# Kernel tuning notes

Measured on AMD Instinct MI355X. Metric: run time of the kernel, lower is better.

Reference implementation:

```python
import jax, jax.numpy as jnp
import numpy as np
from jax import lax

INPUT_SIZE = 16384
NUM_CONV = 128
KMAX = 11  # max kernel size from {7, 9, 11}
BATCH = 256


def setup_inputs() -> dict:
    # Mirror FeatureExtractor._generate_random_params / _generate_random_convolutions
    rng = np.random.RandomState(0)
    kernel_sizes = rng.choice([7, 9, 11], NUM_CONV)
    dilations, paddings = [], []
    W = np.zeros((NUM_CONV, KMAX), np.float32)  # zero-padded kernel bank
    b = np.zeros((NUM_CONV,), np.float32)
    for i, k in enumerate(kernel_sizes):
        d_f = 2.0 ** rng.uniform(0.0, np.log2((INPUT_SIZE - 1) / (k - 1)))
        p = (k - 1) * d_f // 2 if rng.randint(2) else 0
        dilations.append(int(d_f))
        paddings.append(int(p))
        w = rng.normal(0.0, 1.0, k)
        w = w - w.mean()  # centered kernel ('normal' sampling type)
        W[i, :k] = w.astype(np.float32)
        b[i] = rng.uniform(-1.0, 1.0)
    key = jax.random.key(0)
    x = jax.random.normal(key, (BATCH, 1, INPUT_SIZE), dtype=jnp.float32)
    return {
        "x": x,
        "weights": jnp.asarray(W),
        "biases": jnp.asarray(b),
        "kernel_sizes": np.asarray(kernel_sizes, np.int64),
        "dilations": np.asarray(dilations, np.int64),
        "paddings": np.asarray(paddings, np.int64),
    }


def reference(x, weights, biases, kernel_sizes, dilations, paddings):
    # x: [B, 1, L]. Each conv has its own (k, dilation, padding) -> distinct
    # output lengths, so a Python loop over the fixed NUM_CONV structurally
    # distinct convs is required (matches the original module).
    feats = []
    n = weights.shape[0]
    for i in range(n):
        k = int(kernel_sizes[i])
        d = int(dilations[i])
        p = int(paddings[i])
        w = weights[i, :k].reshape(1, 1, k)  # OIW
        # torch Conv1d = cross-correlation with rhs (kernel) dilation
        y = lax.conv_general_dilated(
            x, w, window_strides=(1,), padding=[(p, p)], rhs_dilation=(d,)
        ) + biases[i]
        fm = y[:, 0, :]                      # [B, L_out]
        mx = fm.max(axis=-1)                 # global max pool
        ppv = (fm >= 0).sum(axis=-1) / fm.shape[-1]  # proportion of positives
        feats.append(jnp.stack([mx, ppv.astype(x.dtype)], axis=-1))  # [B, 2]
    out = jnp.concatenate(feats, axis=-1)    # [B, 2*num_conv], interleaved (max, ppv)
    return out.reshape(out.shape[0], 1, out.shape[1])  # [B, 1, 2*num_conv]
```

## Files before the change

kernel.cpp:

```cpp
#include <hip/hip_runtime.h>
#include <math.h>

#define S_LEN   16384
#define NCONV   128
#define NBATCH  256
#define TPB     1024
#define NGRP    8
#define DSTRIDE 24
#define BIGQ    (1 << 28)
#define CLMP    65552u

typedef float __attribute__((address_space(1))) as1_float;
typedef float __attribute__((address_space(3))) as3_float;
typedef __attribute__((ext_vector_type(2))) float f2;
typedef unsigned long long u64;

__global__ void setup_desc(const int* __restrict__ ks, const int* __restrict__ dil,
                           const int* __restrict__ pad, const float* __restrict__ W,
                           const float* __restrict__ bias, int* __restrict__ ws)
{
  __shared__ int cost_s[NCONV];
  __shared__ int grp_s[NCONV];
  const int ci = threadIdx.x;
  const int is64 = (ks[1] == 0);
  const int k = is64 ? ks[2 * ci]  : ks[ci];
  const int d = is64 ? dil[2 * ci] : dil[ci];
  const int p = is64 ? pad[2 * ci] : pad[ci];
  const int L = S_LEN + 2 * p - d * (k - 1);
  const int A = L / d, B = L - A * d;
  int cost = L * (k + 5) + ((d >= 128) ? (d >> 1) : 64) * (k - 1) * 2;
  if (d == 1) cost = L * (k + 5) * 2;
  cost_s[ci] = cost;
  __syncthreads();
  int rank = 0;
  for (int j = 0; j < NCONV; ++j) {
    const int cj = cost_s[j];
    rank += (cj > cost) || (cj == cost && j < ci);
  }
  int gg = rank & 7;
  if ((rank >> 3) & 1) gg = 7 - gg;
  grp_s[ci] = gg;
  __syncthreads();
  int rho = 0;
  for (int j = 0; j < NCONV; ++j) {
    if (grp_s[j] != gg) continue;
    const int cj = cost_s[j];
    rho += (cj > cost) || (cj == cost && j < ci);
  }
#pragma unroll
  for (int h = 0; h < 2; ++h) {
    const int j2 = 2 * rho + h;
    const int wv = (j2 < 16) ? j2 : 31 - j2;
    const int sq = (j2 < 16) ? 0 : 1;
    int* dsc = ws + (gg * 32 + wv * 2 + sq) * DSTRIDE;
    dsc[0] = d; dsc[1] = p; dsc[2] = A; dsc[3] = B;
    dsc[4] = ci; dsc[5] = rho; dsc[6] = h; dsc[7] = k;
    ((float*)dsc)[8] = 1.0f / (float)L;
    ((float*)dsc)[9] = bias[ci];
#pragma unroll
    for (int t = 0; t < 11; ++t) ((float*)dsc)[10 + t] = W[ci * 11 + t];
  }
}

__device__ __forceinline__ float sgpr_f(float v) {
  return __int_as_float(__builtin_amdgcn_readfirstlane(__float_as_int(v)));
}
__device__ __forceinline__ int sgpr_i(int v) {
  return __builtin_amdgcn_readfirstlane(v);
}
__device__ __forceinline__ float rcpf(float x) { return __builtin_amdgcn_rcpf(x); }

__device__ __forceinline__ int divq(int num, float rd, int d) {
  int q = (int)((float)num * rd);
  q -= (q * d > num);
  q += ((q + 1) * d <= num);
  return q;
}

__device__ __forceinline__ f2 rd2b(const float* sh, int ib) {
  unsigned u = (unsigned)ib;
  u = u > CLMP ? CLMP : u;
  const float* p = (const float*)((const char*)sh + u);
  f2 v; v.x = p[0]; v.y = p[1];
  return v;
}
__device__ __forceinline__ float ld1b(const float* sh, int ib) {
  unsigned u = (unsigned)ib;
  u = u > CLMP ? CLMP : u;
  return *(const float*)((const char*)sh + u);
}

__device__ __forceinline__ f2 pfma(f2 a, f2 b, f2 c) {
#if __has_builtin(__builtin_elementwise_fma)
  return __builtin_elementwise_fma(a, b, c);
#else
  f2 r; r.x = fmaf(a.x, b.x, c.x); r.y = fmaf(a.y, b.y, c.y); return r;
#endif
}
__device__ __forceinline__ f2 pmax(f2 a, f2 b) {
#if __has_builtin(__builtin_elementwise_max)
  return __builtin_elementwise_max(a, b);
#else
  f2 r; r.x = fmaxf(a.x, b.x); r.y = fmaxf(a.y, b.y); return r;
#endif
}
__device__ __forceinline__ int wcount(bool pred) {
  return (int)__popcll(__ballot(pred));
}

template <int K>
__device__ __forceinline__ void pwalk(
    const float* sh, const u64* wu, const f2 bbv,
    int d, int sb4, int q0, int q1, f2& mxv, int& cw)
{
  const int n = q1 - q0;
  if (n <= 0) return;
  f2 win[K];
  int bb = (sb4 + q0 * d) * 4;
#pragma unroll
  for (int t = 0; t < K - 1; ++t)
    win[t] = rd2b(sh, bb + t * (d * 4));
  bb += (K - 1) * (d * 4);
  int i = 0;
  for (; i + K <= n; i += K) {
#pragma unroll
    for (int s = 0; s < K; ++s) {
      const f2 cur = rd2b(sh, bb + s * (d * 4));
      f2 a = pfma(__builtin_bit_cast(f2, wu[0]), win[s % K], bbv);
#pragma unroll
      for (int t = 1; t < K; ++t)
        a = pfma(__builtin_bit_cast(f2, wu[t]),
                 (t == K - 1) ? cur : win[(s + t) % K], a);
      win[(s + K - 1) % K] = cur;
      mxv = pmax(mxv, a);
      cw += wcount(a.x >= 0.f);
      cw += wcount(a.y >= 0.f);
    }
    bb += K * (d * 4);
  }
  const int rem = n - i;
  if (rem > 0) {
#pragma unroll
    for (int s = 0; s < K - 1; ++s) {
      const f2 cur = rd2b(sh, bb + s * (d * 4));
      f2 a = pfma(__builtin_bit_cast(f2, wu[0]), win[s % K], bbv);
#pragma unroll
      for (int t = 1; t < K; ++t)
        a = pfma(__builtin_bit_cast(f2, wu[t]),
                 (t == K - 1) ? cur : win[(s + t) % K], a);
      win[(s + K - 1) % K] = cur;
      const bool ok = (s < rem);
      if (ok) mxv = pmax(mxv, a);
      cw += wcount(ok && (a.x >= 0.f));
      cw += wcount(ok && (a.y >= 0.f));
    }
  }
}

template <int K>
__device__ __forceinline__ void swalk(
    const float* sh, const float* w, float bval,
    int d, int sb4, int q0, int q1, float& mx, int& cw)
{
  const int n = q1 - q0;
  if (n <= 0) return;
  float win[K];
  int bb = (sb4 + q0 * d) * 4;
#pragma unroll
  for (int t = 0; t < K - 1; ++t)
    win[t] = ld1b(sh, bb + t * (d * 4));
  bb += (K - 1) * (d * 4);
  int i = 0;
  for (; i + K <= n; i += K) {
#pragma unroll
    for (int s = 0; s < K; ++s) {
      const float cur = ld1b(sh, bb + s * (d * 4));
      float a = fmaf(w[0], win[s % K], bval);
#pragma unroll
      for (int t = 1; t < K; ++t)
        a = fmaf(w[t], (t == K - 1) ? cur : win[(s + t) % K], a);
      win[(s + K - 1) % K] = cur;
      mx = fmaxf(mx, a);
      cw += wcount(a >= 0.f);
    }
    bb += K * (d * 4);
  }
  const int rem = n - i;
  if (rem > 0) {
#pragma unroll
    for (int s = 0; s < K - 1; ++s) {
      const float cur = ld1b(sh, bb + s * (d * 4));
      float a = fmaf(w[0], win[s % K], bval);
#pragma unroll
      for (int t = 1; t < K; ++t)
        a = fmaf(w[t], (t == K - 1) ? cur : win[(s + t) % K], a);
      win[(s + K - 1) % K] = cur;
      const bool ok = (s < rem);
      if (ok) mx = fmaxf(mx, a);
      cw += wcount(ok && (a >= 0.f));
    }
  }
}

template <int K>
__device__ __forceinline__ void scalar_split(
    const float* sh, const float* w, float bval,
    int d, int p, int r, int c0, int c1, int lane, float& mx, int& cw)
{
  const int n = c1 - c0;
  if (n <= 0) return;
  const int v  = lane;
  const int mm = n >> 6;
  const int sA = (mm >= 32) ? (v & 31) : (((v & 31) * mm) >> 5);
  const int vB = v + 1;
  const int sB = (mm >= 32) ? (vB & 31) : (((vB & 31) * mm) >> 5);
  const int q0 = c0 + (int)(((long long)n * v) >> 6) + sA;
  const int q1 = (v == 63) ? c1 : c0 + (int)(((long long)n * vB) >> 6) + sB;
  swalk<K>(sh, w, bval, d, r - p + 4, q0, q1, mx, cw);
}

template <int K>
__device__ __forceinline__ void one_out(
    const float* sh, const float* w, float bval,
    int d, int p, int j, float& mx, int& cw)
{
  float a = bval;
  int bb = (j - p + 4) * 4;
#pragma unroll
  for (int t = 0; t < K; ++t) { a = fmaf(w[t], ld1b(sh, bb), a); bb += d * 4; }
  mx = fmaxf(mx, a);
  cw += wcount(a >= 0.f);
}

template <int K>
__device__ __forceinline__ void conv_chunk(
    const float* sh, const u64* wu, const float* w, float bval, const f2 bbv,
    int d, int p, int A, int B, int h, int lane,
    f2& mxv, float& mxs, int& cw)
{
  if (d == 1) {
    const int H = (A + 1) >> 1;
    scalar_split<K>(sh, w, bval, 1, p, 0, h ? H : 0, h ? A : H, lane, mxs, cw);
    return;
  }
  const int npair = d >> 1;
  if (npair >= 128) {
    const int half = npair >> 1;
    const int g0 = h ? half : 0;
    const int g1 = h ? npair : half;
    for (int c = g0 + lane; c < g1; c += 64) {
      const int r0 = 2 * c;
      const int Qm = A + (r0 + 1 < B);
      pwalk<K>(sh, wu, bbv, d, r0 - p + 4, 0, Qm, mxv, cw);
      if (B == r0 + 1) one_out<K>(sh, w, bval, d, p, r0 + A * d, mxs, cw);
    }
  } else if (npair >= 64) {
    const int H = (A + 1) >> 1;
    const int c0 = h ? H : 0;
    const int c1 = h ? BIGQ : H;
    for (int c = lane; c < npair; c += 64) {
      const int r0 = 2 * c;
      const int Qm = A + (r0 + 1 < B);
      pwalk<K>(sh, wu, bbv, d, r0 - p + 4, c0, min(c1, Qm), mxv, cw);
      if (B == r0 + 1 && A >= c0 && A < c1)
        one_out<K>(sh, w, bval, d, p, r0 + A * d, mxs, cw);
    }
  } else {
    const int H = (A + 1) >> 1;
    const int c0 = h ? H : 0;
    const int c1h = h ? BIGQ : H;
    const float rdp = rcpf((float)npair);
    int v  = (int)((float)lane * rdp);
    int g2 = lane - v * npair;
    if (g2 < 0)           { --v; g2 += npair; }
    else if (g2 >= npair) { ++v; g2 -= npair; }
    const int nv = divq(63 - g2, rdp, npair) + 1;
    const int r0 = 2 * g2;
    const int Qm = A + (r0 + 1 < B);
    const int cc1 = min(c1h, Qm);
    const int n = cc1 - c0;
    if (n > 0) {
      const float rn = rcpf((float)nv);
      const int mm = (int)((float)n * rn);
      const int sA = (mm >= 32) ? (v & 31) : (((v & 31) * mm) >> 5);
      const int vB = v + 1;
      const int sB = (mm >= 32) ? (vB & 31) : (((vB & 31) * mm) >> 5);
      const int q0 = c0 + (int)((float)(n * v) * rn) + sA;
      const int q1 = (v == nv - 1) ? cc1
                   : c0 + (int)((float)(n * vB) * rn) + sB;
      pwalk<K>(sh, wu, bbv, d, r0 - p + 4, q0, q1, mxv, cw);
    }
    if (v == nv - 1 && B == r0 + 1 && A >= c0 && A < c1h)
      one_out<K>(sh, w, bval, d, p, r0 + A * d, mxs, cw);
  }
  if ((d & 1) && d > 1) {
    const int H2 = (A + 1) >> 1;
    const int r = d - 1;
    const int Qr = A + (r < B);
    const int c0 = h ? H2 : 0;
    const int c1 = h ? Qr : min(H2, Qr);
    scalar_split<K>(sh, w, bval, d, p, r, c0, c1, lane, mxs, cw);
  }
}

__global__ __launch_bounds__(TPB, 8) void rocket_feats(
    const float* __restrict__ x, const int* __restrict__ ws,
    float* __restrict__ out)
{
  __shared__ float sh[S_LEN + 8];
  __shared__ float smx[2][16];
  __shared__ int   scn[2][16];
  __shared__ int   sci[16];
  __shared__ float sin_[16];

  const int tid  = threadIdx.x;
  const int blk  = blockIdx.x;
  const int g    = blk & 7;
  const int b    = blk >> 3;
  const int lane = tid & 63, wid = tid >> 6;

  const float* xrow = x + (size_t)b * S_LEN;
  {
    const float* gb = xrow + lane * 4;
#pragma unroll
    for (int c = 0; c < 4; ++c) {
      const int off = (wid * 4 + c) * 256;
      __builtin_amdgcn_global_load_lds((const as1_float*)(gb + off),
                                       (as3_float*)(sh + 4 + off), 16, 0, 0);
    }
  }
  if (tid < 4) sh[tid] = 0.f;
  if (tid >= 4 && tid < 8) sh[S_LEN + tid] = 0.f;
  __syncthreads();

  for (int sq = 0; sq < 2; ++sq) {
    const int* dsc = ws + (g * 32 + wid * 2 + sq) * DSTRIDE;
    const int d  = sgpr_i(dsc[0]);
    const int p  = sgpr_i(dsc[1]);
    const int A  = sgpr_i(dsc[2]);
    const int B  = sgpr_i(dsc[3]);
    const int ci = sgpr_i(dsc[4]);
    const int t_ = sgpr_i(dsc[5]);
    const int h  = sgpr_i(dsc[6]);
    const int k  = sgpr_i(dsc[7]);
    const float invL = sgpr_f(((const float*)dsc)[8]);
    const float bval = sgpr_f(((const float*)dsc)[9]);
    float wf[11]; u64 wu[11];
#pragma unroll
    for (int t = 0; t < 11; ++t) {
      wf[t] = sgpr_f(((const float*)dsc)[10 + t]);
      const unsigned wb = (unsigned)__float_as_int(wf[t]);
      wu[t] = ((u64)wb << 32) | (u64)wb;
    }
    f2 bbv; bbv.x = bval; bbv.y = bval;

    f2 mxv; mxv.x = -INFINITY; mxv.y = -INFINITY;
    float mxs = -INFINITY;
    int cw = 0;

    if (k == 7)
      conv_chunk<7 >(sh, wu, wf, bval, bbv, d, p, A, B, h, lane, mxv, mxs, cw);
    else if (k == 9)
      conv_chunk<9 >(sh, wu, wf, bval, bbv, d, p, A, B, h, lane, mxv, mxs, cw);
    else
      conv_chunk<11>(sh, wu, wf, bval, bbv, d, p, A, B, h, lane, mxv, mxs, cw);

    float mx = fmaxf(fmaxf(mxv.x, mxv.y), mxs);
#pragma unroll
    for (int off = 32; off > 0; off >>= 1)
      mx = fmaxf(mx, __shfl_down(mx, off, 64));
    if (lane == 0) {
      smx[h][t_] = mx; scn[h][t_] = cw;
      sci[t_] = ci; sin_[t_] = invL;
    }
  }

  __syncthreads();
  if (tid < 16) {
    const float m = fmaxf(smx[0][tid], smx[1][tid]);
    const int   c = scn[0][tid] + scn[1][tid];
    out[(size_t)b * (2 * NCONV) + 2 * sci[tid]]     = m;
    out[(size_t)b * (2 * NCONV) + 2 * sci[tid] + 1] = (float)c * sin_[tid];
  }
}

extern "C" void kernel_launch(void* const* d_in, const int* in_sizes, int n_in,
                              void* d_out, int out_size, void* d_ws, size_t ws_size,
                              hipStream_t stream) {
  const float* x    = (const float*)d_in[0];
  const float* W    = (const float*)d_in[1];
  const float* bias = (const float*)d_in[2];
  const int*   ks   = (const int*)d_in[3];
  const int*   dil  = (const int*)d_in[4];
  const int*   pad  = (const int*)d_in[5];
  float* out = (float*)d_out;
  int*   ws  = (int*)d_ws;

  hipLaunchKernelGGL(setup_desc, dim3(1), dim3(NCONV), 0, stream,
                     ks, dil, pad, W, bias, ws);
  hipLaunchKernelGGL(rocket_feats, dim3(NBATCH * NGRP), dim3(TPB), 0, stream,
                     x, ws, out);
}
```

Baseline: 272.6 us.

## Process four dilated residue streams per lane with quad walk

Replaces the pair-of-residues walk for dilated convolutions with a quad walk that computes four adjacent residue streams per lane using two packed-FMA accumulators. It adds a pair/scalar split for the leftover residues and for dilations 2 and 3, and updates the cost model used for load balancing. The aim is to amortize LDS address computation and loop overhead over more outputs and to raise ILP. In exchange it doubles register pressure for the sliding windows, which could hurt occupancy, and it changes how work is divided across lanes for mid-range dilations.

New measurement: 316.1 us. 15.9% more time.

```diff
diff --git a/kernel.cpp b/kernel.cpp
--- a/kernel.cpp
+++ b/kernel.cpp
@@ -28,8 +28,8 @@
   const int p = is64 ? pad[2 * ci] : pad[ci];
   const int L = S_LEN + 2 * p - d * (k - 1);
   const int A = L / d, B = L - A * d;
-  int cost = L * (k + 5) + ((d >= 128) ? (d >> 1) : 64) * (k - 1) * 2;
-  if (d == 1) cost = L * (k + 5) * 2;
+  int cost = L * (k + 5) + ((d >= 512) ? (d >> 2) : 64) * (k - 1) * 4;
+  if (d < 4) cost = L * (k + 5) * 2;
   cost_s[ci] = cost;
   __syncthreads();
   int rank = 0;
@@ -158,8 +158,76 @@
 }
 
 template <int K>
+__device__ __forceinline__ void qwalk(
+    const float* sh, const u64* wu, const f2 bbv,
+    int d, int sb4, int q0, int q1, f2& mxv, int& cw)
+{
+  const int n = q1 - q0;
+  if (n <= 0) return;
+  f2 wlo[K], whi[K];
+  int bb = (sb4 + q0 * d) * 4;
+#pragma unroll
+  for (int t = 0; t < K - 1; ++t) {
+    wlo[t] = rd2b(sh, bb + t * (d * 4));
+    whi[t] = rd2b(sh, bb + t * (d * 4) + 8);
+  }
+  bb += (K - 1) * (d * 4);
+  int i = 0;
+  for (; i + K <= n; i += K) {
+#pragma unroll
+    for (int s = 0; s < K; ++s) {
+      const f2 clo = rd2b(sh, bb + s * (d * 4));
+      const f2 chi = rd2b(sh, bb + s * (d * 4) + 8);
+      f2 alo = pfma(__builtin_bit_cast(f2, wu[0]), wlo[s % K], bbv);
+      f2 ahi = pfma(__builtin_bit_cast(f2, wu[0]), whi[s % K], bbv);
+#pragma unroll
+      for (int t = 1; t < K; ++t) {
+        alo = pfma(__builtin_bit_cast(f2, wu[t]),
+                   (t == K - 1) ? clo : wlo[(s + t) % K], alo);
+        ahi = pfma(__builtin_bit_cast(f2, wu[t]),
+                   (t == K - 1) ? chi : whi[(s + t) % K], ahi);
+      }
+      wlo[(s + K - 1) % K] = clo;
+      whi[(s + K - 1) % K] = chi;
+      mxv = pmax(mxv, alo);
+      mxv = pmax(mxv, ahi);
+      cw += wcount(alo.x >= 0.f);
+      cw += wcount(alo.y >= 0.f);
+      cw += wcount(ahi.x >= 0.f);
+      cw += wcount(ahi.y >= 0.f);
+    }
+    bb += K * (d * 4);
+  }
+  const int rem = n - i;
+  if (rem > 0) {
+#pragma unroll
+    for (int s = 0; s < K - 1; ++s) {
+      const f2 clo = rd2b(sh, bb + s * (d * 4));
+      const f2 chi = rd2b(sh, bb + s * (d * 4) + 8);
+      f2 alo = pfma(__builtin_bit_cast(f2, wu[0]), wlo[s % K], bbv);
+      f2 ahi = pfma(__builtin_bit_cast(f2, wu[0]), whi[s % K], bbv);
+#pragma unroll
+      for (int t = 1; t < K; ++t) {
+        alo = pfma(__builtin_bit_cast(f2, wu[t]),
+                   (t == K - 1) ? clo : wlo[(s + t) % K], alo);
+        ahi = pfma(__builtin_bit_cast(f2, wu[t]),
+                   (t == K - 1) ? chi : whi[(s + t) % K], ahi);
+      }
+      wlo[(s + K - 1) % K] = clo;
+      whi[(s + K - 1) % K] = chi;
+      const bool ok = (s < rem);
+      if (ok) { mxv = pmax(mxv, alo); mxv = pmax(mxv, ahi); }
+      cw += wcount(ok && (alo.x >= 0.f));
+      cw += wcount(ok && (alo.y >= 0.f));
+      cw += wcount(ok && (ahi.x >= 0.f));
+      cw += wcount(ok && (ahi.y >= 0.f));
+    }
+  }
+}
+
+template <int K>
 __device__ __forceinline__ void swalk(
-    const float* sh, const float* w, float bval,
+    const float* sh, const float* wf, float bval,
     int d, int sb4, int q0, int q1, float& mx, int& cw)
 {
   const int n = q1 - q0;
@@ -175,10 +243,10 @@
 #pragma unroll
     for (int s = 0; s < K; ++s) {
       const float cur = ld1b(sh, bb + s * (d * 4));
-      float a = fmaf(w[0], win[s % K], bval);
+      float a = fmaf(wf[0], win[s % K], bval);
 #pragma unroll
       for (int t = 1; t < K; ++t)
-        a = fmaf(w[t], (t == K - 1) ? cur : win[(s + t) % K], a);
+        a = fmaf(wf[t], (t == K - 1) ? cur : win[(s + t) % K], a);
       win[(s + K - 1) % K] = cur;
       mx = fmaxf(mx, a);
       cw += wcount(a >= 0.f);
@@ -190,10 +258,10 @@
 #pragma unroll
     for (int s = 0; s < K - 1; ++s) {
       const float cur = ld1b(sh, bb + s * (d * 4));
-      float a = fmaf(w[0], win[s % K], bval);
+      float a = fmaf(wf[0], win[s % K], bval);
 #pragma unroll
       for (int t = 1; t < K; ++t)
-        a = fmaf(w[t], (t == K - 1) ? cur : win[(s + t) % K], a);
+        a = fmaf(wf[t], (t == K - 1) ? cur : win[(s + t) % K], a);
       win[(s + K - 1) % K] = cur;
       const bool ok = (s < rem);
       if (ok) mx = fmaxf(mx, a);
@@ -204,7 +272,7 @@
 
 template <int K>
 __device__ __forceinline__ void scalar_split(
-    const float* sh, const float* w, float bval,
+    const float* sh, const float* wf, float bval,
     int d, int p, int r, int c0, int c1, int lane, float& mx, int& cw)
 {
   const int n = c1 - c0;
@@ -216,67 +284,106 @@
   const int sB = (mm >= 32) ? (vB & 31) : (((vB & 31) * mm) >> 5);
   const int q0 = c0 + (int)(((long long)n * v) >> 6) + sA;
   const int q1 = (v == 63) ? c1 : c0 + (int)(((long long)n * vB) >> 6) + sB;
-  swalk<K>(sh, w, bval, d, r - p + 4, q0, q1, mx, cw);
+  swalk<K>(sh, wf, bval, d, r - p + 4, q0, q1, mx, cw);
+}
+
+template <int K>
+__device__ __forceinline__ void pair_split(
+    const float* sh, const u64* wu, const f2 bbv,
+    int d, int p, int r, int c0, int c1, int lane, f2& mxv, int& cw)
+{
+  const int n = c1 - c0;
+  if (n <= 0) return;
+  const int v  = lane;
+  const int mm = n >> 6;
+  const int sA = (mm >= 32) ? (v & 31) : (((v & 31) * mm) >> 5);
+  const int vB = v + 1;
+  const int sB = (mm >= 32) ? (vB & 31) : (((vB & 31) * mm) >> 5);
+  const int q0 = c0 + (int)(((long long)n * v) >> 6) + sA;
+  const int q1 = (v == 63) ? c1 : c0 + (int)(((long long)n * vB) >> 6) + sB;
+  pwalk<K>(sh, wu, bbv, d, r - p + 4, q0, q1, mxv, cw);
 }
 
 template <int K>
 __device__ __forceinline__ void one_out(
-    const float* sh, const float* w, float bval,
+    const float* sh, const float* wf, float bval,
     int d, int p, int j, float& mx, int& cw)
 {
   float a = bval;
   int bb = (j - p + 4) * 4;
 #pragma unroll
-  for (int t = 0; t < K; ++t) { a = fmaf(w[t], ld1b(sh, bb), a); bb += d * 4; }
+  for (int t = 0; t < K; ++t) { a = fmaf(wf[t], ld1b(sh, bb), a); bb += d * 4; }
   mx = fmaxf(mx, a);
   cw += wcount(a >= 0.f);
 }
 
 template <int K>
 __device__ __forceinline__ void conv_chunk(
-    const float* sh, const u64* wu, const float* w, float bval, const f2 bbv,
+    const float* sh, const u64* wu, const float* wf, float bval, const f2 bbv,
     int d, int p, int A, int B, int h, int lane,
     f2& mxv, float& mxs, int& cw)
 {
   if (d == 1) {
     const int H = (A + 1) >> 1;
-    scalar_split<K>(sh, w, bval, 1, p, 0, h ? H : 0, h ? A : H, lane, mxs, cw);
+    scalar_split<K>(sh, wf, bval, 1, p, 0, h ? H : 0, h ? A : H, lane, mxs, cw);
     return;
   }
-  const int npair = d >> 1;
-  if (npair >= 128) {
-    const int half = npair >> 1;
+  if (d < 4) {
+    const int H = (A + 1) >> 1;
+    const int Qm = A + (1 < B);
+    pair_split<K>(sh, wu, bbv, d, p, 0, h ? H : 0, h ? Qm : H, lane, mxv, cw);
+    if (h && lane == 63 && B == 1)
+      one_out<K>(sh, wf, bval, d, p, A * d, mxs, cw);
+    if (d == 3) {
+      const int Qr = A + (2 < B);
+      scalar_split<K>(sh, wf, bval, d, p, 2, h ? H : 0, h ? Qr : min(H, Qr),
+                      lane, mxs, cw);
+    }
+    return;
+  }
+  const int nq = d >> 2;
+  if (nq >= 128) {
+    const int half = nq >> 1;
     const int g0 = h ? half : 0;
-    const int g1 = h ? npair : half;
+    const int g1 = h ? nq : half;
     for (int c = g0 + lane; c < g1; c += 64) {
-      const int r0 = 2 * c;
-      const int Qm = A + (r0 + 1 < B);
-      pwalk<K>(sh, wu, bbv, d, r0 - p + 4, 0, Qm, mxv, cw);
-      if (B == r0 + 1) one_out<K>(sh, w, bval, d, p, r0 + A * d, mxs, cw);
-    }
-  } else if (npair >= 64) {
+      const int r0 = 4 * c;
+      const int Qm = A + (r0 + 3 < B);
+      qwalk<K>(sh, wu, bbv, d, r0 - p + 4, 0, Qm, mxv, cw);
+      if (r0 + 3 >= B) {
+#pragma unroll
+        for (int j = 0; j < 3; ++j)
+          if (r0 + j < B)
+            one_out<K>(sh, wf, bval, d, p, r0 + j + A * d, mxs, cw);
+      }
+    }
+  } else if (nq >= 64) {
     const int H = (A + 1) >> 1;
     const int c0 = h ? H : 0;
     const int c1 = h ? BIGQ : H;
-    for (int c = lane; c < npair; c += 64) {
-      const int r0 = 2 * c;
-      const int Qm = A + (r0 + 1 < B);
-      pwalk<K>(sh, wu, bbv, d, r0 - p + 4, c0, min(c1, Qm), mxv, cw);
-      if (B == r0 + 1 && A >= c0 && A < c1)
-        one_out<K>(sh, w, bval, d, p, r0 + A * d, mxs, cw);
+    for (int c = lane; c < nq; c += 64) {
+      const int r0 = 4 * c;
+      const int Qm = A + (r0 + 3 < B);
+      qwalk<K>(sh, wu, bbv, d, r0 - p + 4, c0, min(c1, Qm), mxv, cw);
+      if (r0 + 3 >= B && A >= c0 && A < c1) {
+#pragma unroll
+        for (int j = 0; j < 3; ++j)
+          if (r0 + j < B)
+            one_out<K>(sh, wf, bval, d, p, r0 + j + A * d, mxs, cw);
+      }
     }
   } else {
     const int H = (A + 1) >> 1;
     const int c0 = h ? H : 0;
     const int c1h = h ? BIGQ : H;
-    const float rdp = rcpf((float)npair);
+    const float rdp = rcpf((float)nq);
     int v  = (int)((float)lane * rdp);
-    int g2 = lane - v * npair;
-    if (g2 < 0)           { --v; g2 += npair; }
-    else if (g2 >= npair) { ++v; g2 -= npair; }
-    const int nv = divq(63 - g2, rdp, npair) + 1;
-    const int r0 = 2 * g2;
-    const int Qm = A + (r0 + 1 < B);
+    int g2 = lane - v * nq;
+    if (g2 < 0)         { --v; g2 += nq; }
+    else if (g2 >= nq)  { ++v; g2 -= nq; }
+    const int nv = divq(63 - g2, rdp, nq) + 1;
+    const int r0 = 4 * g2;
+    const int Qm = A + (r0 + 3 < B);
     const int cc1 = min(c1h, Qm);
     const int n = cc1 - c0;
     if (n > 0) {
@@ -288,18 +395,32 @@
       const int q0 = c0 + (int)((float)(n * v) * rn) + sA;
       const int q1 = (v == nv - 1) ? cc1
                    : c0 + (int)((float)(n * vB) * rn) + sB;
-      pwalk<K>(sh, wu, bbv, d, r0 - p + 4, q0, q1, mxv, cw);
-    }
-    if (v == nv - 1 && B == r0 + 1 && A >= c0 && A < c1h)
-      one_out<K>(sh, w, bval, d, p, r0 + A * d, mxs, cw);
-  }
-  if ((d & 1) && d > 1) {
-    const int H2 = (A + 1) >> 1;
-    const int r = d - 1;
-    const int Qr = A + (r < B);
-    const int c0 = h ? H2 : 0;
-    const int c1 = h ? Qr : min(H2, Qr);
-    scalar_split<K>(sh, w, bval, d, p, r, c0, c1, lane, mxs, cw);
+      qwalk<K>(sh, wu, bbv, d, r0 - p + 4, q0, q1, mxv, cw);
+    }
+    if (v == nv - 1 && r0 + 3 >= B && A >= c0 && A < c1h) {
+#pragma unroll
+      for (int j = 0; j < 3; ++j)
+        if (r0 + j < B)
+          one_out<K>(sh, wf, bval, d, p, r0 + j + A * d, mxs, cw);
+    }
+  }
+  const int rem = d & 3;
+  if (rem) {
+    const int H = (A + 1) >> 1;
+    if (rem >= 2) {
+      const int r = d - rem;
+      const int Qm = A + (r + 1 < B);
+      pair_split<K>(sh, wu, bbv, d, p, r, h ? H : 0, h ? Qm : min(H, Qm),
+                    lane, mxv, cw);
+      if (h && lane == 63 && B == r + 1)
+        one_out<K>(sh, wf, bval, d, p, r + A * d, mxs, cw);
+    }
+    if (rem & 1) {
+      const int r = d - 1;
+      const int Qr = A + (r < B);
+      scalar_split<K>(sh, wf, bval, d, p, r, h ? H : 0, h ? Qr : min(H, Qr),
+                      lane, mxs, cw);
+    }
   }
 }
 
```
